# Optimization experiments

Hardware: AMD Instinct MI355X
Metric: run time of the kernel (lower is better)

The kernel has to match this reference:

```python
import jax, jax.numpy as jnp
import numpy as np

B, C, DD, HH, WW = 1, 128, 16, 16, 16
D_STATE, D_CONV, EXPAND = 16, 4, 2
D_INNER = EXPAND * C
DT_RANK = (C + 15) // 16


def setup_inputs():
    key = jax.random.key(0)
    ks = jax.random.split(key, 10)
    def w(k, shape, s=0.02):
        return jax.random.normal(k, shape, dtype=jnp.float32) * s
    return {
        "x": jax.random.normal(ks[0], (B, C, DD, HH, WW), dtype=jnp.float32),
        "ln_w": jnp.ones((C,), jnp.float32),
        "ln_b": jnp.zeros((C,), jnp.float32),
        "mnorm_w": jnp.ones((C,), jnp.float32),
        "mnorm_b": jnp.zeros((C,), jnp.float32),
        "in_proj_w": w(ks[1], (2 * D_INNER, C)),
        "conv_w": w(ks[2], (D_INNER, D_CONV), 0.2),
        "conv_b": jnp.zeros((D_INNER,), jnp.float32),
        "x_proj_w": w(ks[3], (DT_RANK + 2 * D_STATE, D_INNER)),
        "dt_proj_w": w(ks[4], (D_INNER, DT_RANK), 0.1),
        "dt_proj_b": jnp.full((D_INNER,), float(np.log(np.expm1(0.01))), jnp.float32),
        "A_log": jnp.log(jnp.tile(jnp.arange(1, D_STATE + 1, dtype=jnp.float32), (D_INNER, 1))),
        "D_param": jnp.ones((D_INNER,), jnp.float32),
        "out_proj_w": w(ks[5], (C, D_INNER)),
        "proj_w": w(ks[6], (C, 3 * C)),
        "proj_b": jnp.zeros((C,), jnp.float32),
        "fc1_w": w(ks[7], (4 * C, C)),
        "fc1_b": jnp.zeros((4 * C,), jnp.float32),
        "fc2_w": w(ks[8], (C, 4 * C)),
        "fc2_b": jnp.zeros((C,), jnp.float32),
    }


def _ln_cf(x, w, b, eps=1e-6):
    # channels_first LayerNorm over axis 1 (matches custom LayerNorm)
    u = x.mean(1, keepdims=True)
    s = ((x - u) ** 2).mean(1, keepdims=True)
    xn = (x - u) * jax.lax.rsqrt(s + eps)
    return w[None, :, None, None, None] * xn + b[None, :, None, None, None]


def _ln_last(x, w, b, eps=1e-5):
    u = x.mean(-1, keepdims=True)
    s = ((x - u) ** 2).mean(-1, keepdims=True)
    return (x - u) * jax.lax.rsqrt(s + eps) * w + b


def _selective_scan(u, delta, A, Bm, Cm, Dv):
    # u, delta: (N,L,d); Bm,Cm: (N,L,n); A: (d,n); Dv: (d,)
    dA = jnp.exp(delta[..., None] * A)                               # (N,L,d,n)
    dBu = delta[..., None] * Bm[:, :, None, :] * u[..., None]         # (N,L,d,n)
    def step(h, inp):
        dA_t, dBu_t, C_t = inp
        h = dA_t * h + dBu_t
        y = jnp.einsum("bdn,bn->bd", h, C_t)
        return h, y
    h0 = jnp.zeros((u.shape[0], A.shape[0], A.shape[1]), u.dtype)
    _, ys = jax.lax.scan(step, h0, (dA.swapaxes(0, 1), dBu.swapaxes(0, 1), Cm.swapaxes(0, 1)))
    return ys.swapaxes(0, 1) + u * Dv


def _mamba(xin, in_proj_w, conv_w, conv_b, x_proj_w, dt_proj_w, dt_proj_b, A_log, D_param, out_proj_w):
    # xin: (N, L, C)
    N, L, _ = xin.shape
    xz = xin @ in_proj_w.T                                            # (N,L,2*d_inner)
    xr, z = jnp.split(xz, 2, axis=-1)
    # causal depthwise conv1d, kernel D_CONV, left-padded (mamba conv1d[..., :L])
    xp = jnp.pad(xr, ((0, 0), (D_CONV - 1, 0), (0, 0)))
    xc = sum(conv_w[:, k] * xp[:, k:k + L, :] for k in range(D_CONV)) + conv_b
    xc = jax.nn.silu(xc)
    x_dbl = xc @ x_proj_w.T                                           # (N,L,dt_rank+2n)
    dt = x_dbl[..., :DT_RANK]
    Bm = x_dbl[..., DT_RANK:DT_RANK + D_STATE]
    Cm = x_dbl[..., DT_RANK + D_STATE:]
    delta = jax.nn.softplus(dt @ dt_proj_w.T + dt_proj_b)
    A = -jnp.exp(A_log)
    y = _selective_scan(xc, delta, A, Bm, Cm, D_param)
    y = y * jax.nn.silu(z)
    return y @ out_proj_w.T


def _forward(x, ln_w, ln_b, mnorm_w, mnorm_b, in_proj_w, conv_w, conv_b, x_proj_w, dt_proj_w, dt_proj_b, A_log, D_param, out_proj_w, proj_w, proj_b, fc1_w, fc1_b, fc2_w, fc2_b):
    Bb, Cc, Dd, Hh, Ww = x.shape
    L = Dd * Hh * Ww
    x1 = _ln_cf(x, ln_w, ln_b)
    # three directional flattenings (d-, h-, w-major); cube => shapes identical
    xd = x1.reshape(Bb, Cc, L)
    xh = x1.transpose(0, 1, 3, 4, 2).reshape(Bb, Cc, L)
    xw = x1.transpose(0, 1, 4, 2, 3).reshape(Bb, Cc, L)
    seq = jnp.stack([xd, xh, xw], 0).reshape(3 * Bb, Cc, L).swapaxes(1, 2)  # (3B,L,C)
    seq = _ln_last(seq, mnorm_w, mnorm_b)
    y = _mamba(seq, in_proj_w, conv_w, conv_b, x_proj_w, dt_proj_w, dt_proj_b, A_log, D_param, out_proj_w)
    # reassemble per-direction volumes (no inverse permute, matching torch code) and concat on channels
    cat = y.swapaxes(1, 2).reshape(3, Bb, Cc, Dd, Hh, Ww).transpose(1, 0, 2, 3, 4, 5).reshape(Bb, 3 * Cc, Dd, Hh, Ww)
    out1 = jnp.einsum("bkdhw,ok->bodhw", cat, proj_w) + proj_b[None, :, None, None, None]
    out_res = x + out1
    h = _ln_cf(out_res, ln_w, ln_b)
    h = jnp.einsum("bcdhw,oc->bodhw", h, fc1_w) + fc1_b[None, :, None, None, None]
    h = jax.nn.gelu(h, approximate=False)
    h = jnp.einsum("bcdhw,oc->bodhw", h, fc2_w) + fc2_b[None, :, None, None, None]
    return h + out_res


def reference(x, ln_w, ln_b, mnorm_w, mnorm_b, in_proj_w, conv_w, conv_b, x_proj_w, dt_proj_w, dt_proj_b, A_log, D_param, out_proj_w, proj_w, proj_b, fc1_w, fc1_b, fc2_w, fc2_b):
    return _forward(x, ln_w, ln_b, mnorm_w, mnorm_b, in_proj_w, conv_w, conv_b, x_proj_w, dt_proj_w, dt_proj_b, A_log, D_param, out_proj_w, proj_w, proj_b, fc1_w, fc1_b, fc2_w, fc2_b)
```

## Files before the change

### kernel.cpp

```cpp
#include <hip/hip_runtime.h>
#include <hip/hip_bf16.h>
#include <math.h>

#define L 4096
#define C 128
#define DI 256
#define NST 16
#define NS 3
#define NCH 256
#define CT 16
#define R3 12288

typedef unsigned short u16;

__device__ __forceinline__ float siluf(float x){ return x / (1.f + __expf(-x)); }
__device__ __forceinline__ float geluf(float x){ return 0.5f*x*(1.f + erff(x*0.70710678118654752f)); }

__device__ __forceinline__ float b2f(u16 h){ return __uint_as_float(((unsigned)h)<<16); }
__device__ __forceinline__ u16 f2b(float f){
  unsigned u = __float_as_uint(f);
  return (u16)((u + 0x7FFFu + ((u>>16)&1u)) >> 16);
}
__device__ __forceinline__ float4 b4f(const u16* p){
  ushort4 v = *(const ushort4*)p;
  return make_float4(b2f(v.x), b2f(v.y), b2f(v.z), b2f(v.w));
}
__device__ __forceinline__ float2 b2f2(const u16* p){
  ushort2 v = *(const ushort2*)p;
  return make_float2(b2f(v.x), b2f(v.y));
}
__device__ __forceinline__ ushort2 f2b2(float a, float b){
  ushort2 r; r.x = f2b(a); r.y = f2b(b); return r;
}

__device__ __forceinline__ int permf(int s, int l){
  if(s==0) return l;
  if(s==1) return ((l&15)<<8) | ((l>>8)<<4) | ((l>>4)&15);
  return (((l>>4)&15)<<8) | ((l&15)<<4) | (l>>8);
}

__global__ void k_front(const float* __restrict__ x, const float* __restrict__ lw,
                        const float* __restrict__ lb, const float* __restrict__ mw,
                        const float* __restrict__ mb, const float* __restrict__ ipw,
                        const float* __restrict__ opw, const float* __restrict__ pw,
                        u16* __restrict__ Zb, float* __restrict__ Mw){
  __shared__ float As[128][68];
  __shared__ float Bs[64][132];
  int bid = blockIdx.x;
  int tid = threadIdx.x;
  if(bid < 384){
    int o = bid & 127, s = bid >> 7;
    float acc = 0.f;
    for(int c=0;c<C;c++) acc += opw[c*DI + tid] * pw[o*384 + s*128 + c];
    Mw[(s*256+tid)*128 + o] = acc;
    return;
  }
  int b2 = bid - 384;
  int p0 = (b2 & 63)*64, j0 = (b2 >> 6)*64;
  for(int q=0;q<8;q++){
    int f = q*1024 + tid*4; int cc = f>>6, p = f&63;
    float4 v = *(const float4*)&x[cc*L + p0 + p];
    *(float4*)&As[cc][p] = v;
  }
  for(int q=0;q<8;q++){
    int f = q*1024 + tid*4; int j = f>>7, k = f&127;
    float4 b = *(const float4*)&ipw[(j0+j)*C + k];
    *(float4*)&Bs[j][k] = b;
  }
  __syncthreads();
  {
    int p = tid>>2, kg = tid&3;
    float s=0.f, sq=0.f;
    #pragma unroll
    for(int i=0;i<32;i++){
      int k = kg*32 + ((i + kg*2)&31);
      float v = As[k][p]; s += v; sq += v*v;
    }
    s  += __shfl_xor(s,1);  s  += __shfl_xor(s,2);
    sq += __shfl_xor(sq,1); sq += __shfl_xor(sq,2);
    float m1 = s*(1.f/C);
    float r1 = rsqrtf(sq*(1.f/C) - m1*m1 + 1e-6f);
    float s2=0.f, sq2=0.f;
    #pragma unroll
    for(int i=0;i<32;i++){
      int k = kg*32 + ((i + kg*2)&31);
      float t = lw[k]*((As[k][p]-m1)*r1) + lb[k];
      s2 += t; sq2 += t*t;
    }
    s2  += __shfl_xor(s2,1);  s2  += __shfl_xor(s2,2);
    sq2 += __shfl_xor(sq2,1); sq2 += __shfl_xor(sq2,2);
    float m2 = s2*(1.f/C);
    float r2 = rsqrtf(sq2*(1.f/C) - m2*m2 + 1e-5f);
    #pragma unroll
    for(int i=0;i<32;i++){
      int k = kg*32 + ((i + kg*2)&31);
      float t = lw[k]*((As[k][p]-m1)*r1) + lb[k];
      As[k][p] = mw[k]*((t-m2)*r2) + mb[k];
    }
  }
  __syncthreads();
  int og = tid & 15, r4 = tid >> 4;
  float acc[4][4] = {};
  for(int k=0;k<128;k++){
    float4 av = *(const float4*)&As[k][r4*4];
    float a[4] = {av.x, av.y, av.z, av.w};
    float b[4];
    #pragma unroll
    for(int j=0;j<4;j++) b[j] = Bs[og+16*j][k];
    #pragma unroll
    for(int i=0;i<4;i++)
      #pragma unroll
      for(int j=0;j<4;j++) acc[i][j] += a[i]*b[j];
  }
  #pragma unroll
  for(int i=0;i<4;i++)
    #pragma unroll
    for(int j=0;j<4;j++)
      Zb[(p0+r4*4+i)*512 + j0 + og + 16*j] = f2b(acc[i][j]);
}

__global__ void k_conv2(const u16* __restrict__ Zb, const float* __restrict__ cw,
                        const float* __restrict__ cb, u16* __restrict__ xcb){
  int bl = blockIdx.x;
  int s = bl >> 8, l0 = (bl & 255)*16;
  int t = threadIdx.x;
  int d0 = t*2;
  float w00=cw[d0*4+0], w01=cw[d0*4+1], w02=cw[d0*4+2], w03=cw[d0*4+3];
  float w10=cw[d0*4+4], w11=cw[d0*4+5], w12=cw[d0*4+6], w13=cw[d0*4+7];
  float bb0=cb[d0], bb1=cb[d0+1];
  float2 h0 = make_float2(0.f,0.f), h1 = h0, h2 = h0;
  if(l0 > 0){
    h0 = b2f2(&Zb[permf(s,l0-3)*512 + d0]);
    h1 = b2f2(&Zb[permf(s,l0-2)*512 + d0]);
    h2 = b2f2(&Zb[permf(s,l0-1)*512 + d0]);
  }
  #pragma unroll 4
  for(int st=0; st<16; st++){
    int l = l0 + st;
    float2 cur = b2f2(&Zb[permf(s,l)*512 + d0]);
    float o0 = bb0 + w00*h0.x + w01*h1.x + w02*h2.x + w03*cur.x;
    float o1 = bb1 + w10*h0.y + w11*h1.y + w12*h2.y + w13*cur.y;
    *(ushort2*)&xcb[(s*L + l)*DI + d0] = f2b2(siluf(o0), siluf(o1));
    h0 = h1; h1 = h2; h2 = cur;
  }
}

__global__ void k_xd5(const u16* __restrict__ xcb, const float* __restrict__ xpw,
                      const float* __restrict__ dtw, const float* __restrict__ dtb,
                      float* __restrict__ Bc, float* __restrict__ Cc,
                      u16* __restrict__ deltab){
  __shared__ float As[32][132];
  __shared__ float Ws[40][132];
  __shared__ float BCs[40][33];
  int r0 = blockIdx.x*32;
  int tid = threadIdx.x;
  int r = tid & 31, cg = tid >> 5;
  float acc[5] = {0.f,0.f,0.f,0.f,0.f};
  for(int ph=0; ph<2; ph++){
    int k0 = ph*128;
    for(int q=0;q<4;q++){
      int f = q*256 + tid; int rr = f>>5, kk = (f&31)*4;
      float4 v = b4f(&xcb[(r0+rr)*DI + k0 + kk]);
      *(float4*)&As[rr][kk] = v;
    }
    for(int q=0;q<5;q++){
      int f = q*256 + tid; int col = f>>5, kk = (f&31)*4;
      float4 v = *(const float4*)&xpw[col*DI + k0 + kk];
      *(float4*)&Ws[col][kk] = v;
    }
    __syncthreads();
    for(int k4=0;k4<32;k4++){
      float4 a = *(const float4*)&As[r][k4*4];
      #pragma unroll
      for(int j=0;j<5;j++){
        float4 w = *(const float4*)&Ws[cg*5+j][k4*4];
        acc[j] += a.x*w.x + a.y*w.y + a.z*w.z + a.w*w.w;
      }
    }
    __syncthreads();
  }
  #pragma unroll
  for(int j=0;j<5;j++) BCs[cg*5+j][r] = acc[j];
  __syncthreads();
  {
    float4 ww0 = *(const float4*)&dtw[tid*8];
    float4 ww1 = *(const float4*)&dtw[tid*8+4];
    float bb = dtb[tid];
    #pragma unroll 4
    for(int rr=0;rr<32;rr++){
      float aa = bb + BCs[0][rr]*ww0.x + BCs[1][rr]*ww0.y + BCs[2][rr]*ww0.z + BCs[3][rr]*ww0.w
                    + BCs[4][rr]*ww1.x + BCs[5][rr]*ww1.y + BCs[6][rr]*ww1.z + BCs[7][rr]*ww1.w;
      float dl = (aa > 20.f) ? aa : log1pf(__expf(aa));
      deltab[(r0+rr)*DI + tid] = f2b(dl);
    }
  }
  if(tid < 128){
    int rr = tid>>2, ng = (tid&3)*4;
    float4 bv = make_float4(BCs[ 8+ng][rr], BCs[ 9+ng][rr], BCs[10+ng][rr], BCs[11+ng][rr]);
    *(float4*)&Bc[(r0+rr)*NST + ng] = bv;
  } else {
    int t2 = tid - 128;
    int rr = t2>>2, ng = (t2&3)*4;
    float4 cv = make_float4(BCs[24+ng][rr], BCs[25+ng][rr], BCs[26+ng][rr], BCs[27+ng][rr]);
    *(float4*)&Cc[(r0+rr)*NST + ng] = cv;
  }
}

__global__ void k_scanA(const u16* __restrict__ deltab, const u16* __restrict__ xcb,
                        const float* __restrict__ Bc, const float* __restrict__ A_log,
                        u16* __restrict__ aggAb, u16* __restrict__ aggBb){
  int b = blockIdx.x;
  int ng = b & 3, ch = (b>>2)&255, s = b>>10;
  int d = threadIdx.x;
  int n0 = ng*4;
  float Aa[4], P[4] = {1.f,1.f,1.f,1.f}, S[4] = {0.f,0.f,0.f,0.f};
  #pragma unroll
  for(int j=0;j<4;j++) Aa[j] = -__expf(A_log[d*NST + n0 + j]);
  int base = s*L + ch*CT;
  #pragma unroll
  for(int st=0; st<CT; st++){
    int row = base + st;
    float dl = b2f(deltab[row*DI + d]);
    float u  = b2f(xcb[row*DI + d]);
    float4 bv = *(const float4*)&Bc[row*NST + n0];
    float dlu = dl*u;
    float a;
    a = __expf(dl*Aa[0]); S[0] = a*S[0] + dlu*bv.x; P[0] *= a;
    a = __expf(dl*Aa[1]); S[1] = a*S[1] + dlu*bv.y; P[1] *= a;
    a = __expf(dl*Aa[2]); S[2] = a*S[2] + dlu*bv.z; P[2] *= a;
    a = __expf(dl*Aa[3]); S[3] = a*S[3] + dlu*bv.w; P[3] *= a;
  }
  int idx0 = ch*R3 + s*256 + d;
  #pragma unroll
  for(int j=0;j<4;j++){
    int idx = idx0 + (n0+j)*768;
    aggAb[idx] = f2b(P[j]); aggBb[idx] = f2b(S[j]);
  }
}

__global__ void k_scanB(const u16* __restrict__ aggAb, const u16* __restrict__ aggBb,
                        u16* __restrict__ hInb){
  __shared__ float PA[32][9], PB[32][9];
  int tid = threadIdx.x;
  int jl = tid & 31, seg = tid >> 5;
  int j = blockIdx.x*32 + jl;
  int c0 = seg*32;
  float pa[32], pb[32];
  float P = 1.f, S = 0.f;
  #pragma unroll
  for(int i=0;i<32;i++){
    pa[i] = P; pb[i] = S;
    float a = b2f(aggAb[(c0+i)*R3 + j]), b = b2f(aggBb[(c0+i)*R3 + j]);
    S = a*S + b; P = a*P;
  }
  PA[jl][seg] = P; PB[jl][seg] = S;
  __syncthreads();
  if(tid < 32){
    float h = 0.f;
    #pragma unroll
    for(int sg=0; sg<8; sg++){
      float p = PA[tid][sg], s2 = PB[tid][sg];
      PA[tid][sg] = h;
      h = p*h + s2;
    }
  }
  __syncthreads();
  float h0 = PA[jl][seg];
  #pragma unroll
  for(int i=0;i<32;i++){
    hInb[(c0+i)*R3 + j] = f2b(pa[i]*h0 + pb[i]);
  }
}

__global__ void k_scanC(const u16* __restrict__ deltab, const u16* __restrict__ xcb,
                        const float* __restrict__ Bc, const float* __restrict__ Cc,
                        const float* __restrict__ A_log, const float* __restrict__ Dp,
                        const u16* __restrict__ Zb, const u16* __restrict__ hInb,
                        u16* __restrict__ yzb){
  int b = blockIdx.x;
  int ch = b & 255, s = b >> 8;
  int d = threadIdx.x;
  float Aa[16], h[16];
  #pragma unroll
  for(int n=0;n<16;n++) Aa[n] = -__expf(A_log[d*NST + n]);
  #pragma unroll
  for(int n=0;n<16;n++) h[n] = b2f(hInb[ch*R3 + n*768 + s*256 + d]);
  float Dv = Dp[d];
  int base = s*L + ch*CT;
  #pragma unroll 2
  for(int st=0; st<CT; st++){
    int row = base + st;
    float dl = b2f(deltab[row*DI + d]);
    float u  = b2f(xcb[row*DI + d]);
    float dlu = dl*u;
    const float4* Bp = (const float4*)&Bc[row*NST];
    const float4* Cp = (const float4*)&Cc[row*NST];
    float y = u*Dv;
    #pragma unroll
    for(int q=0;q<4;q++){
      float4 bv = Bp[q], cv = Cp[q];
      float a;
      a = __expf(dl*Aa[4*q+0]); h[4*q+0] = a*h[4*q+0] + dlu*bv.x; y += h[4*q+0]*cv.x;
      a = __expf(dl*Aa[4*q+1]); h[4*q+1] = a*h[4*q+1] + dlu*bv.y; y += h[4*q+1]*cv.y;
      a = __expf(dl*Aa[4*q+2]); h[4*q+2] = a*h[4*q+2] + dlu*bv.z; y += h[4*q+2]*cv.z;
      a = __expf(dl*Aa[4*q+3]); h[4*q+3] = a*h[4*q+3] + dlu*bv.w; y += h[4*q+3]*cv.w;
    }
    int l = ch*CT + st;
    int p = permf(s, l);
    float zv = b2f(Zb[p*512 + 256 + d]);
    yzb[(s*L + l)*DI + d] = f2b(y * siluf(zv));
  }
}

__global__ void k_proj(const u16* __restrict__ yzb, const float* __restrict__ Mw,
                       u16* __restrict__ ppb){
  __shared__ float As[64][68];
  __shared__ float Bs[64][132];
  int p0 = blockIdx.x*64; int kc = blockIdx.y;
  int s = kc >> 1, d0 = (kc & 1)*128;
  int tid = threadIdx.x;
  int og = tid & 15, r4 = tid >> 4;
  float acc[4][8] = {};
  for(int kk=0; kk<2; kk++){
    int kb = d0 + kk*64;
    for(int q=0;q<4;q++){
      int f = q*256 + tid; int r = f>>4, k = (f&15)*4;
      float4 a = b4f(&yzb[(s*L + p0 + r)*DI + kb + k]);
      *(float4*)&As[r][k] = a;
    }
    for(int q=0;q<8;q++){
      int f = q*1024 + tid*4; int k = f>>7, o = f&127;
      float4 b = *(const float4*)&Mw[(s*256 + kb + k)*128 + o];
      *(float4*)&Bs[k][o] = b;
    }
    __syncthreads();
    for(int k=0;k<64;k++){
      float a[4];
      #pragma unroll
      for(int i=0;i<4;i++) a[i] = As[r4*4+i][k];
      #pragma unroll
      for(int j=0;j<8;j++){
        float bb = Bs[k][og+16*j];
        #pragma unroll
        for(int i=0;i<4;i++) acc[i][j] += a[i]*bb;
      }
    }
    __syncthreads();
  }
  u16* dst = ppb + kc*524288;
  #pragma unroll
  for(int i=0;i<4;i++)
    #pragma unroll
    for(int j=0;j<8;j++)
      dst[(p0+r4*4+i)*C + og + 16*j] = f2b(acc[i][j]);
}

__global__ void k_pred(const u16* __restrict__ ppb, const float* __restrict__ x,
                       const float* __restrict__ pb, float* __restrict__ ores){
  __shared__ float Xs[16][129];
  int p0 = blockIdx.x*16; int tid = threadIdx.x;
  for(int q=0;q<8;q++){
    int f = q*256 + tid; int pl = f&15, o = f>>4;
    Xs[pl][o] = x[o*L + p0 + pl];
  }
  __syncthreads();
  for(int q=0;q<8;q++){
    int f = q*256 + tid; int o = f&127, pl = f>>7;
    int idx = (p0+pl)*C + o;
    float v = b2f(ppb[idx]) + b2f(ppb[524288+idx]) + b2f(ppb[1048576+idx])
            + b2f(ppb[1572864+idx]) + b2f(ppb[2097152+idx]) + b2f(ppb[2621440+idx]);
    ores[idx] = v + Xs[pl][o] + pb[o];
  }
}

__global__ void k_fc1(const float* __restrict__ ores, const float* __restrict__ lw,
                      const float* __restrict__ lb, const float* __restrict__ w1,
                      const float* __restrict__ b1, u16* __restrict__ Hb){
  __shared__ float As[64][129];
  __shared__ float Bs[64][129];
  int p0 = blockIdx.x*64, j0 = blockIdx.y*64;
  int tid = threadIdx.x;
  for(int q=0;q<8;q++){
    int f = q*1024 + tid*4; int r = f>>7, k = f&127;
    float4 a = *(const float4*)&ores[(p0+r)*C + k];
    As[r][k]=a.x; As[r][k+1]=a.y; As[r][k+2]=a.z; As[r][k+3]=a.w;
    float4 b = *(const float4*)&w1[(j0+r)*C + k];
    Bs[r][k]=b.x; Bs[r][k+1]=b.y; Bs[r][k+2]=b.z; Bs[r][k+3]=b.w;
  }
  __syncthreads();
  {
    int r = tid>>2, kg = tid&3;
    float s=0.f, sq=0.f;
    #pragma unroll
    for(int i=0;i<32;i++){
      int k = kg*32 + ((i + kg*8)&31);
      float v = As[r][k]; s += v; sq += v*v;
    }
    s  += __shfl_xor(s,1);  s  += __shfl_xor(s,2);
    sq += __shfl_xor(sq,1); sq += __shfl_xor(sq,2);
    float m1 = s*(1.f/C);
    float r1 = rsqrtf(sq*(1.f/C) - m1*m1 + 1e-6f);
    #pragma unroll
    for(int i=0;i<32;i++){
      int k = kg*32 + ((i + kg*8)&31);
      As[r][k] = lw[k]*((As[r][k]-m1)*r1) + lb[k];
    }
  }
  __syncthreads();
  int og = tid & 15, r4 = tid >> 4;
  float acc[4][4] = {};
  for(int k=0;k<128;k++){
    float a[4], b[4];
    #pragma unroll
    for(int i=0;i<4;i++) a[i] = As[r4*4+i][k];
    #pragma unroll
    for(int j=0;j<4;j++) b[j] = Bs[og+16*j][k];
    #pragma unroll
    for(int i=0;i<4;i++)
      #pragma unroll
      for(int j=0;j<4;j++) acc[i][j] += a[i]*b[j];
  }
  #pragma unroll
  for(int i=0;i<4;i++)
    #pragma unroll
    for(int j=0;j<4;j++){
      int jj = j0 + og + 16*j;
      Hb[(p0+r4*4+i)*512 + jj] = f2b(geluf(acc[i][j] + b1[jj]));
    }
}

__global__ void k_fc2(const u16* __restrict__ Hb, const float* __restrict__ w2,
                      u16* __restrict__ fpb){
  __shared__ float As[64][68];
  __shared__ float Bs[128][68];
  int p0 = blockIdx.x*64; int kc = blockIdx.y;
  int tid = threadIdx.x;
  int og = tid & 15, r4 = tid >> 4;
  float acc[4][8] = {};
  for(int kk=0; kk<2; kk++){
    int kb = kc*128 + kk*64;
    for(int q=0;q<4;q++){
      int f = q*256 + tid; int r = f>>4, k = (f&15)*4;
      float4 a = b4f(&Hb[(p0+r)*512 + kb + k]);
      *(float4*)&As[r][k] = a;
    }
    for(int q=0;q<8;q++){
      int f = q*1024 + tid*4; int o = f>>6, k = f&63;
      float4 b = *(const float4*)&w2[o*512 + kb + k];
      *(float4*)&Bs[o][k] = b;
    }
    __syncthreads();
    for(int k=0;k<64;k++){
      float a[4];
      #pragma unroll
      for(int i=0;i<4;i++) a[i] = As[r4*4+i][k];
      #pragma unroll
      for(int j=0;j<8;j++){
        float bb = Bs[og+16*j][k];
        #pragma unroll
        for(int i=0;i<4;i++) acc[i][j] += a[i]*bb;
      }
    }
    __syncthreads();
  }
  u16* dst = fpb + kc*524288;
  #pragma unroll
  for(int i=0;i<4;i++)
    #pragma unroll
    for(int j=0;j<8;j++)
      dst[(p0+r4*4+i)*C + og + 16*j] = f2b(acc[i][j]);
}

__global__ void k_fred(const u16* __restrict__ fpb, const float* __restrict__ b2,
                       const float* __restrict__ ores, float* __restrict__ out){
  __shared__ float S[128][17];
  int p0 = blockIdx.x*16; int tid = threadIdx.x;
  for(int q=0;q<8;q++){
    int f = q*256 + tid; int o = f&127, pl = f>>7;
    int idx = (p0+pl)*C + o;
    float v = b2f(fpb[idx]) + b2f(fpb[524288+idx]) + b2f(fpb[1048576+idx]) + b2f(fpb[1572864+idx]);
    S[o][pl] = v + b2[o] + ores[idx];
  }
  __syncthreads();
  for(int q=0;q<8;q++){
    int f = q*256 + tid; int pl = f&15, o = f>>4;
    out[o*L + p0 + pl] = S[o][pl];
  }
}

extern "C" void kernel_launch(void* const* d_in, const int* in_sizes, int n_in,
                              void* d_out, int out_size, void* d_ws, size_t ws_size,
                              hipStream_t stream) {
  const float* x     = (const float*)d_in[0];
  const float* ln_w  = (const float*)d_in[1];
  const float* ln_b  = (const float*)d_in[2];
  const float* mw    = (const float*)d_in[3];
  const float* mb    = (const float*)d_in[4];
  const float* ipw   = (const float*)d_in[5];
  const float* cw    = (const float*)d_in[6];
  const float* cb    = (const float*)d_in[7];
  const float* xpw   = (const float*)d_in[8];
  const float* dtw   = (const float*)d_in[9];
  const float* dtb   = (const float*)d_in[10];
  const float* A_log = (const float*)d_in[11];
  const float* Dp    = (const float*)d_in[12];
  const float* opw   = (const float*)d_in[13];
  const float* pw    = (const float*)d_in[14];
  const float* pb    = (const float*)d_in[15];
  const float* w1    = (const float*)d_in[16];
  const float* b1    = (const float*)d_in[17];
  const float* w2    = (const float*)d_in[18];
  const float* b2    = (const float*)d_in[19];
  float* out = (float*)d_out;

  char* wsb = (char*)d_ws;
  u16* Zb     = (u16*)(wsb);
  u16* xcb    = (u16*)(wsb +  4194304);
  u16* deltab = (u16*)(wsb + 10485760);
  u16* aggAb  = (u16*)(wsb + 16777216);
  u16* aggBb  = (u16*)(wsb + 23068672);
  u16* hInb   = (u16*)(wsb + 29360128);
  float* Bc   = (float*)(wsb + 35651584);
  float* Cc   = (float*)(wsb + 36438016);
  float* Mw   = (float*)(wsb + 37224448);
  float* ores = (float*)(wsb + 37617664);
  u16* yzb = aggAb;
  u16* ppb = deltab;
  u16* Hb  = Zb;
  u16* fpb = xcb;

  k_front <<<896, 256, 0, stream>>>(x, ln_w, ln_b, mw, mb, ipw, opw, pw, Zb, Mw);
  k_conv2 <<<768, 128, 0, stream>>>(Zb, cw, cb, xcb);
  k_xd5   <<<384, 256, 0, stream>>>(xcb, xpw, dtw, dtb, Bc, Cc, deltab);
  k_scanA <<<3072, 256, 0, stream>>>(deltab, xcb, Bc, A_log, aggAb, aggBb);
  k_scanB <<<384, 256, 0, stream>>>(aggAb, aggBb, hInb);
  k_scanC <<<768, 256, 0, stream>>>(deltab, xcb, Bc, Cc, A_log, Dp, Zb, hInb, yzb);
  k_proj  <<<dim3(64,6), 256, 0, stream>>>(yzb, Mw, ppb);
  k_pred  <<<256, 256, 0, stream>>>(ppb, x, pb, ores);
  k_fc1   <<<dim3(64,8), 256, 0, stream>>>(ores, ln_w, ln_b, w1, b1, Hb);
  k_fc2   <<<dim3(64,4), 256, 0, stream>>>(Hb, w2, fpb);
  k_fred  <<<256, 256, 0, stream>>>(fpb, b2, ores, out);
}
```

Measured before the change: 260.2 us.

## Split x_proj GEMM over K into two blocks with separate reduce-and-dt kernel

The fused x_proj + dt_proj kernel is split in two. The first kernel runs the K=256 reduction as two independent halves across a second grid dimension and writes partial sums to a new fp32 workspace. The second kernel adds the halves, applies dt_proj and softplus, and writes B/C on 16-row tiles with twice as many blocks. This raises block-level parallelism for the 384-block GEMM, at the cost of an extra launch and a round trip of partial results through global memory.

```diff
diff --git a/kernel.cpp b/kernel.cpp
--- a/kernel.cpp
+++ b/kernel.cpp
@@ -145,63 +145,71 @@
   }
 }
 
-__global__ void k_xd5(const u16* __restrict__ xcb, const float* __restrict__ xpw,
-                      const float* __restrict__ dtw, const float* __restrict__ dtb,
-                      float* __restrict__ Bc, float* __restrict__ Cc,
-                      u16* __restrict__ deltab){
+__global__ void k_xd4a(const u16* __restrict__ xcb, const float* __restrict__ xpw,
+                       float* __restrict__ xp){
   __shared__ float As[32][132];
   __shared__ float Ws[40][132];
-  __shared__ float BCs[40][33];
   int r0 = blockIdx.x*32;
-  int tid = threadIdx.x;
+  int k0 = blockIdx.y*128;
+  int tid = threadIdx.x;
+  for(int q=0;q<4;q++){
+    int f = q*256 + tid; int r = f>>5, kk = (f&31)*4;
+    float4 v = b4f(&xcb[(r0+r)*DI + k0 + kk]);
+    *(float4*)&As[r][kk] = v;
+  }
+  for(int q=0;q<5;q++){
+    int f = q*256 + tid; int col = f>>5, kk = (f&31)*4;
+    float4 v = *(const float4*)&xpw[col*DI + k0 + kk];
+    *(float4*)&Ws[col][kk] = v;
+  }
+  __syncthreads();
   int r = tid & 31, cg = tid >> 5;
   float acc[5] = {0.f,0.f,0.f,0.f,0.f};
-  for(int ph=0; ph<2; ph++){
-    int k0 = ph*128;
-    for(int q=0;q<4;q++){
-      int f = q*256 + tid; int rr = f>>5, kk = (f&31)*4;
-      float4 v = b4f(&xcb[(r0+rr)*DI + k0 + kk]);
-      *(float4*)&As[rr][kk] = v;
-    }
-    for(int q=0;q<5;q++){
-      int f = q*256 + tid; int col = f>>5, kk = (f&31)*4;
-      float4 v = *(const float4*)&xpw[col*DI + k0 + kk];
-      *(float4*)&Ws[col][kk] = v;
-    }
-    __syncthreads();
-    for(int k4=0;k4<32;k4++){
-      float4 a = *(const float4*)&As[r][k4*4];
-      #pragma unroll
-      for(int j=0;j<5;j++){
-        float4 w = *(const float4*)&Ws[cg*5+j][k4*4];
-        acc[j] += a.x*w.x + a.y*w.y + a.z*w.z + a.w*w.w;
-      }
-    }
-    __syncthreads();
-  }
-  #pragma unroll
-  for(int j=0;j<5;j++) BCs[cg*5+j][r] = acc[j];
+  for(int k4=0;k4<32;k4++){
+    float4 a = *(const float4*)&As[r][k4*4];
+    #pragma unroll
+    for(int j=0;j<5;j++){
+      float4 w = *(const float4*)&Ws[cg*5+j][k4*4];
+      acc[j] += a.x*w.x + a.y*w.y + a.z*w.z + a.w*w.w;
+    }
+  }
+  float* dst = xp + (blockIdx.y*12288 + r0 + r)*40 + cg*5;
+  #pragma unroll
+  for(int j=0;j<5;j++) dst[j] = acc[j];
+}
+
+__global__ void k_xd4b(const float* __restrict__ xp, const float* __restrict__ dtw,
+                       const float* __restrict__ dtb, float* __restrict__ Bc,
+                       float* __restrict__ Cc, u16* __restrict__ deltab){
+  __shared__ float xdb[40][17];
+  int r0 = blockIdx.x*16;
+  int tid = threadIdx.x;
+  for(int e=tid; e<640; e+=256){
+    int row = e/40, col = e%40;
+    int idx = (r0+row)*40 + col;
+    xdb[col][row] = xp[idx] + xp[491520 + idx];
+  }
   __syncthreads();
   {
     float4 ww0 = *(const float4*)&dtw[tid*8];
     float4 ww1 = *(const float4*)&dtw[tid*8+4];
     float bb = dtb[tid];
     #pragma unroll 4
-    for(int rr=0;rr<32;rr++){
-      float aa = bb + BCs[0][rr]*ww0.x + BCs[1][rr]*ww0.y + BCs[2][rr]*ww0.z + BCs[3][rr]*ww0.w
-                    + BCs[4][rr]*ww1.x + BCs[5][rr]*ww1.y + BCs[6][rr]*ww1.z + BCs[7][rr]*ww1.w;
+    for(int r=0;r<16;r++){
+      float aa = bb + xdb[0][r]*ww0.x + xdb[1][r]*ww0.y + xdb[2][r]*ww0.z + xdb[3][r]*ww0.w
+                    + xdb[4][r]*ww1.x + xdb[5][r]*ww1.y + xdb[6][r]*ww1.z + xdb[7][r]*ww1.w;
       float dl = (aa > 20.f) ? aa : log1pf(__expf(aa));
-      deltab[(r0+rr)*DI + tid] = f2b(dl);
-    }
-  }
-  if(tid < 128){
+      deltab[(r0+r)*DI + tid] = f2b(dl);
+    }
+  }
+  if(tid < 64){
     int rr = tid>>2, ng = (tid&3)*4;
-    float4 bv = make_float4(BCs[ 8+ng][rr], BCs[ 9+ng][rr], BCs[10+ng][rr], BCs[11+ng][rr]);
+    float4 bv = make_float4(xdb[8+ng][rr], xdb[9+ng][rr], xdb[10+ng][rr], xdb[11+ng][rr]);
     *(float4*)&Bc[(r0+rr)*NST + ng] = bv;
-  } else {
-    int t2 = tid - 128;
+  } else if(tid < 128){
+    int t2 = tid - 64;
     int rr = t2>>2, ng = (t2&3)*4;
-    float4 cv = make_float4(BCs[24+ng][rr], BCs[25+ng][rr], BCs[26+ng][rr], BCs[27+ng][rr]);
+    float4 cv = make_float4(xdb[24+ng][rr], xdb[25+ng][rr], xdb[26+ng][rr], xdb[27+ng][rr]);
     *(float4*)&Cc[(r0+rr)*NST + ng] = cv;
   }
 }
@@ -524,6 +532,7 @@
   float* Cc   = (float*)(wsb + 36438016);
   float* Mw   = (float*)(wsb + 37224448);
   float* ores = (float*)(wsb + 37617664);
+  float* xp   = (float*)(wsb + 39714816);
   u16* yzb = aggAb;
   u16* ppb = deltab;
   u16* Hb  = Zb;
@@ -531,7 +540,8 @@
 
   k_front <<<896, 256, 0, stream>>>(x, ln_w, ln_b, mw, mb, ipw, opw, pw, Zb, Mw);
   k_conv2 <<<768, 128, 0, stream>>>(Zb, cw, cb, xcb);
-  k_xd5   <<<384, 256, 0, stream>>>(xcb, xpw, dtw, dtb, Bc, Cc, deltab);
+  k_xd4a  <<<dim3(384,2), 256, 0, stream>>>(xcb, xpw, xp);
+  k_xd4b  <<<768, 256, 0, stream>>>(xp, dtw, dtb, Bc, Cc, deltab);
   k_scanA <<<3072, 256, 0, stream>>>(deltab, xcb, Bc, A_log, aggAb, aggBb);
   k_scanB <<<384, 256, 0, stream>>>(aggAb, aggBb, hInb);
   k_scanC <<<768, 256, 0, stream>>>(deltab, xcb, Bc, Cc, A_log, Dp, Zb, hInb, yzb);
```

New measurement: 251.2 us. -3.5%, faster.
